# Kernel optimization log

Hardware: AMD Instinct MI355X
Metric: run time of the kernel (lower is better)

Reference implementation:

```python
import jax, jax.numpy as jnp
import numpy as np

TEMPERATURE = 11.313708498984761  # sqrt(128)


def setup_inputs() -> dict:
    key = jax.random.key(0)
    kq, kk, kv = jax.random.split(key, 3)
    b, n, m, d, dv = 16, 2048, 2048, 128, 128
    return {
        "queries": jax.random.normal(kq, (b, n, d), dtype=jnp.float32),
        "keys": jax.random.normal(kk, (b, m, d), dtype=jnp.float32),
        "values": jax.random.normal(kv, (b, m, dv), dtype=jnp.float32),
    }


def reference(queries, keys, values):
    # scores: [b, n, m]
    scores = jnp.einsum('bnd,bmd->bnm', queries, keys) / TEMPERATURE
    attn = jax.nn.softmax(scores, axis=2)
    # out: [b, n, d']
    return jnp.einsum('bnm,bmd->bnd', attn, values)
```

## Files before the change

kernel.cpp:

```cpp
#include <hip/hip_runtime.h>


#define BATCH 16
#define SEQ   2048
#define DIM   128
#define NT    (SEQ / 64)

typedef short bf16x8 __attribute__((ext_vector_type(8)));
typedef float f32x16 __attribute__((ext_vector_type(16)));

static __device__ __forceinline__ unsigned pk2(float lo, float hi) {
  union { float f; unsigned u; } a, b;
  a.f = lo; b.f = hi;
  return ((b.u + 0x8000u) & 0xffff0000u) | ((a.u + 0x8000u) >> 16);
}
static __device__ __forceinline__ float fast_exp2(float x) {
#if __has_builtin(__builtin_amdgcn_exp2f)
  return __builtin_amdgcn_exp2f(x);
#else
  return exp2f(x);
#endif
}

typedef __attribute__((address_space(1))) const unsigned int g_u32;
typedef __attribute__((address_space(3))) unsigned int l_u32;
static __device__ __forceinline__ void gl2lds16(const unsigned short* g, unsigned short* l) {
  __builtin_amdgcn_global_load_lds((g_u32*)g, (l_u32*)l, 16, 0, 0);
}

__global__ __launch_bounds__(256)
void prep_kernel(const float* __restrict__ K, const float* __restrict__ V,
                 unsigned short* __restrict__ Kb, unsigned short* __restrict__ Vt,
                 float scale) {
  const int bx = blockIdx.x, tid = threadIdx.x;
  if (bx < 2048) {
    size_t idx = (size_t)bx * 256 + tid;
    const float4* kf = (const float4*)K;
    float4 a = kf[idx * 2], c = kf[idx * 2 + 1];
    uint4 o;
    o.x = pk2(a.x * scale, a.y * scale);
    o.y = pk2(a.z * scale, a.w * scale);
    o.z = pk2(c.x * scale, c.y * scale);
    o.w = pk2(c.z * scale, c.w * scale);
    ((uint4*)Kb)[idx] = o;
  } else {
    __shared__ float tile[128][33];
    const int vb = bx - 2048;
    const int b = vb >> 6, r = vb & 63;
    const int m0 = (r & 15) * 128, d0 = (r >> 4) * 32;
    const int c = tid & 7, mr = tid >> 3;
    const float* src = V + ((size_t)(b * SEQ) + m0) * DIM + d0;
#pragma unroll
    for (int it = 0; it < 4; ++it) {
      int m = it * 32 + mr;
      float4 x = *(const float4*)(src + (size_t)m * DIM + c * 4);
      tile[m][c * 4 + 0] = x.x; tile[m][c * 4 + 1] = x.y;
      tile[m][c * 4 + 2] = x.z; tile[m][c * 4 + 3] = x.w;
    }
    __syncthreads();
    const int dr = tid >> 3, s = tid & 7;
    unsigned short* dst = Vt + ((size_t)(b * DIM) + d0 + dr) * SEQ + m0;
#pragma unroll
    for (int it = 0; it < 2; ++it) {
      int slot = it * 8 + s;
      uint4 o;
      o.x = pk2(tile[slot * 8 + 0][dr], tile[slot * 8 + 1][dr]);
      o.y = pk2(tile[slot * 8 + 2][dr], tile[slot * 8 + 3][dr]);
      o.z = pk2(tile[slot * 8 + 4][dr], tile[slot * 8 + 5][dr]);
      o.w = pk2(tile[slot * 8 + 6][dr], tile[slot * 8 + 7][dr]);
      *(uint4*)(dst + slot * 8) = o;
    }
  }
}


__global__ __launch_bounds__(256, 2)
void attn_kernel(const float* __restrict__ Qf,
                 const unsigned short* __restrict__ Kb,
                 const unsigned short* __restrict__ Vtb,
                 float* __restrict__ out) {
  __shared__ __align__(1024) unsigned char smem[65536];
  unsigned short* sm16 = (unsigned short*)smem;

  const int tid  = threadIdx.x;
  const int wv   = tid >> 6;
  const int w_q  = wv & 1;
  const int w_m  = wv >> 1;
  const int lane = tid & 63;
  const int l31  = lane & 31;
  const int q2   = lane >> 5;
  const int b    = blockIdx.x;
  const int q0   = blockIdx.y * 64 + w_q * 32;

  const unsigned short* kb = Kb  + (size_t)b * SEQ * DIM;
  const unsigned short* vb = Vtb + (size_t)b * SEQ * DIM;

  bf16x8 aq[8];
  {
    const float* qp = Qf + ((size_t)(b * SEQ) + q0 + l31) * DIM + q2 * 8;
#pragma unroll
    for (int c = 0; c < 8; ++c) {
      float4 x = *(const float4*)(qp + c * 16);
      float4 y = *(const float4*)(qp + c * 16 + 4);
      union { unsigned i[4]; bf16x8 v; } u;
      u.i[0] = pk2(x.x, x.y); u.i[1] = pk2(x.z, x.w);
      u.i[2] = pk2(y.x, y.y); u.i[3] = pk2(y.z, y.w);
      aq[c] = u.v;
    }
  }

  unsigned kgo[4], vgo[4];
#pragma unroll
  for (int i = 0; i < 4; ++i) {
    int ch = wv * 4 + i;
    int krow = ch * 4 + (lane >> 4);
    kgo[i] = (unsigned)(krow * 128) + ((((lane & 15) << 4) ^ ((krow & 15) << 4)) >> 1);
    int vrow = ch * 8 + (lane >> 3);
    vgo[i] = (unsigned)(vrow * 2048) + ((((lane & 7) << 4) ^ ((vrow & 7) << 4)) >> 1);
  }

  const int kro = ((w_m * 32 + l31) << 8) + ((q2 << 4) ^ ((l31 & 15) << 4));
  const int vro = (l31 << 7) + (((w_m << 6) + (q2 << 4)) ^ ((l31 & 7) << 4));

  f32x16 oacc[4];
#pragma unroll
  for (int t = 0; t < 4; ++t)
#pragma unroll
    for (int i = 0; i < 16; ++i) oacc[t][i] = 0.0f;
  float ls[4] = {0.0f, 0.0f, 0.0f, 0.0f};

#define STAGE(TK, BUF) do {                                                  \
    const unsigned short* kt_b = kb + ((size_t)(TK) << 13);                  \
    const unsigned short* vt_b = vb + ((TK) << 6);                           \
    unsigned short* kd = sm16 + (((BUF) + wv * 4096) >> 1);                  \
    unsigned short* vd = sm16 + ((32768 + (BUF) + wv * 4096) >> 1);          \
    _Pragma("unroll")                                                        \
    for (int i = 0; i < 4; ++i) gl2lds16(kt_b + kgo[i], kd + i * 512);       \
    _Pragma("unroll")                                                        \
    for (int i = 0; i < 4; ++i) gl2lds16(vt_b + vgo[i], vd + i * 512);       \
  } while (0)

#define VLOAD(CUR) do {                                                      \
    const unsigned char* vB_ = smem + 32768 + (CUR);                         \
    _Pragma("unroll")                                                        \
    for (int t = 0; t < 4; ++t) {                                            \
      vr[2 * t]     = *(const bf16x8*)(vB_ + t * 4096 + vro);                \
      vr[2 * t + 1] = *(const bf16x8*)(vB_ + t * 4096 + (vro ^ 32));         \
    }                                                                        \
  } while (0)

#define QK(CUR, SD) do {                                                     \
    const unsigned char* kB_ = smem + (CUR);                                 \
    f32x16 se, so;                                                           \
    _Pragma("unroll")                                                        \
    for (int i = 0; i < 16; ++i) { se[i] = 0.0f; so[i] = 0.0f; }             \
    __builtin_amdgcn_s_setprio(1);                                           \
    _Pragma("unroll")                                                        \
    for (int c = 0; c < 4; ++c) {                                            \
      bf16x8 b0 = *(const bf16x8*)(kB_ + (kro ^ ((2 * c) << 5)));            \
      se = __builtin_amdgcn_mfma_f32_32x32x16_bf16(b0, aq[2 * c], se, 0, 0, 0); \
      bf16x8 b1 = *(const bf16x8*)(kB_ + (kro ^ ((2 * c + 1) << 5)));        \
      so = __builtin_amdgcn_mfma_f32_32x32x16_bf16(b1, aq[2 * c + 1], so, 0, 0, 0); \
    }                                                                        \
    __builtin_amdgcn_s_setprio(0);                                           \
    _Pragma("unroll")                                                        \
    for (int i = 0; i < 16; ++i) SD[i] = se[i] + so[i];                      \
  } while (0)

#define SOFTMAX(S, PU0, PU1) do {                                            \
    float p[16];                                                             \
    _Pragma("unroll")                                                        \
    for (int i = 0; i < 16; ++i) p[i] = fast_exp2(S[i]);                     \
    _Pragma("unroll")                                                        \
    for (int i = 0; i < 4; ++i) {                                            \
      ls[0] += p[4 * i + 0]; ls[1] += p[4 * i + 1];                          \
      ls[2] += p[4 * i + 2]; ls[3] += p[4 * i + 3];                          \
    }                                                                        \
    unsigned d0, d1, d2, d3, d4, d5, d6, d7;                                 \
    asm("v_cvt_pk_bf16_f32 %0, %1, %2" : "=v"(d0) : "v"(p[0]),  "v"(p[1]));  \
    asm("v_cvt_pk_bf16_f32 %0, %1, %2" : "=v"(d1) : "v"(p[2]),  "v"(p[3]));  \
    asm("v_cvt_pk_bf16_f32 %0, %1, %2" : "=v"(d2) : "v"(p[4]),  "v"(p[5]));  \
    asm("v_cvt_pk_bf16_f32 %0, %1, %2" : "=v"(d3) : "v"(p[6]),  "v"(p[7]));  \
    asm("v_cvt_pk_bf16_f32 %0, %1, %2" : "=v"(d4) : "v"(p[8]),  "v"(p[9]));  \
    asm("v_cvt_pk_bf16_f32 %0, %1, %2" : "=v"(d5) : "v"(p[10]), "v"(p[11])); \
    asm("v_cvt_pk_bf16_f32 %0, %1, %2" : "=v"(d6) : "v"(p[12]), "v"(p[13])); \
    asm("v_cvt_pk_bf16_f32 %0, %1, %2" : "=v"(d7) : "v"(p[14]), "v"(p[15])); \
    asm("v_permlane32_swap_b32 %0, %1" : "+v"(d0), "+v"(d2));                \
    asm("v_permlane32_swap_b32 %0, %1" : "+v"(d1), "+v"(d3));                \
    asm("v_permlane32_swap_b32 %0, %1" : "+v"(d4), "+v"(d6));                \
    asm("v_permlane32_swap_b32 %0, %1" : "+v"(d5), "+v"(d7));                \
    PU0.u[0] = d0; PU0.u[1] = d1; PU0.u[2] = d2; PU0.u[3] = d3;              \
    PU1.u[0] = d4; PU1.u[1] = d5; PU1.u[2] = d6; PU1.u[3] = d7;              \
  } while (0)

#define PV(PU0, PU1) do {                                                    \
    __builtin_amdgcn_s_setprio(1);                                           \
    _Pragma("unroll")                                                        \
    for (int t = 0; t < 4; ++t) {                                            \
      oacc[t] = __builtin_amdgcn_mfma_f32_32x32x16_bf16(PU0.v, vr[2 * t], oacc[t], 0, 0, 0); \
      oacc[t] = __builtin_amdgcn_mfma_f32_32x32x16_bf16(PU1.v, vr[2 * t + 1], oacc[t], 0, 0, 0); \
    }                                                                        \
    __builtin_amdgcn_s_setprio(0);                                           \
  } while (0)

  bf16x8 vr[8];
  f32x16 sA, sB;

  STAGE(0, 0);
  __syncthreads();
  STAGE(1, 16384);
  QK(0, sA);

#pragma unroll 1
  for (int t = 0; t < NT - 2; t += 2) {
    {
      VLOAD(0);
      __syncthreads();
      STAGE(t + 2, 0);
      QK(16384, sB);
      union { unsigned u[4]; bf16x8 v; } pu0, pu1;
      SOFTMAX(sA, pu0, pu1);
      PV(pu0, pu1);
    }
    {
      VLOAD(16384);
      __syncthreads();
      STAGE(t + 3, 16384);
      QK(0, sA);
      union { unsigned u[4]; bf16x8 v; } pu0, pu1;
      SOFTMAX(sB, pu0, pu1);
      PV(pu0, pu1);
    }
  }
  {
    VLOAD(0);
    __syncthreads();
    QK(16384, sB);
    union { unsigned u[4]; bf16x8 v; } pu0, pu1;
    SOFTMAX(sA, pu0, pu1);
    PV(pu0, pu1);
  }
  {
    VLOAD(16384);
    union { unsigned u[4]; bf16x8 v; } pu0, pu1;
    SOFTMAX(sB, pu0, pu1);
    PV(pu0, pu1);
  }

#undef STAGE
#undef VLOAD
#undef QK
#undef SOFTMAX
#undef PV

  float lsum = (ls[0] + ls[1]) + (ls[2] + ls[3]);
  lsum += __shfl_xor(lsum, 32, 64);

  __syncthreads();
  float* cb  = (float*)smem;
  float* cbL = (float*)(smem + 32768);
  if (w_m == 1) {
    float* my = cb + w_q * 4096;
#pragma unroll
    for (int t = 0; t < 4; ++t)
#pragma unroll
      for (int r = 0; r < 16; ++r)
        my[(t * 16 + r) * 64 + lane] = oacc[t][r];
  }
  cbL[w_m * 64 + w_q * 32 + l31] = lsum;
  __syncthreads();
  if (w_m == 0) {
    const float* pr = cb + w_q * 4096;
    float linv[16];
#pragma unroll
    for (int r = 0; r < 16; ++r) {
      int qr = (r & 3) + ((r >> 2) << 3) + (q2 << 2);
      linv[r] = 1.0f / (cbL[w_q * 32 + qr] + cbL[64 + w_q * 32 + qr]);
    }
    float* ob = out + ((size_t)(b * SEQ) + q0) * DIM;
#pragma unroll
    for (int t = 0; t < 4; ++t)
#pragma unroll
      for (int r = 0; r < 16; ++r) {
        int qr = (r & 3) + ((r >> 2) << 3) + (q2 << 2);
        ob[(size_t)qr * DIM + t * 32 + l31] = (oacc[t][r] + pr[(t * 16 + r) * 64 + lane]) * linv[r];
      }
  }
}

extern "C" void kernel_launch(void* const* d_in, const int* in_sizes, int n_in,
                              void* d_out, int out_size, void* d_ws, size_t ws_size,
                              hipStream_t stream) {
  const float* Q = (const float*)d_in[0];
  const float* K = (const float*)d_in[1];
  const float* V = (const float*)d_in[2];
  float* out = (float*)d_out;

  const size_t elems = (size_t)BATCH * SEQ * DIM;
  unsigned short* Kb = (unsigned short*)d_ws;
  unsigned short* Vt = Kb + elems;

  const double TEMPERATURE = 11.313708498984761;
  const float scale = (float)(1.4426950408889634 / TEMPERATURE);

  prep_kernel<<<3072, 256, 0, stream>>>(K, V, Kb, Vt, scale);
  attn_kernel<<<dim3(BATCH, SEQ / 64), 256, 0, stream>>>(Q, Kb, Vt, out);
}
```

Baseline: 137.8 us.

## Load K directly to registers and triple-buffer V in LDS

K fragments are now read straight from global memory into registers per wave instead of being staged through shared memory. Only V is staged, in a three-slot ring that cuts LDS from 64KB to 48KB. The main loop is restructured so PV for the previous tile runs before QK and softmax for the current one, with a raw s_barrier in place of __syncthreads. This removes K traffic through LDS and may allow more occupancy, but it gives up K reuse across waves (each w_q wave reloads K from global), relies on vmcnt being handled correctly without a full __syncthreads, and may lose the overlap of the two-score-buffer pipeline.

```diff
diff --git a/kernel.cpp b/kernel.cpp
--- a/kernel.cpp
+++ b/kernel.cpp
@@ -79,7 +79,7 @@
                  const unsigned short* __restrict__ Kb,
                  const unsigned short* __restrict__ Vtb,
                  float* __restrict__ out) {
-  __shared__ __align__(1024) unsigned char smem[65536];
+  __shared__ __align__(1024) unsigned char smem[49152];
   unsigned short* sm16 = (unsigned short*)smem;
 
   const int tid  = threadIdx.x;
@@ -109,17 +109,15 @@
     }
   }
 
-  unsigned kgo[4], vgo[4];
+  const unsigned short* kwp = kb + ((size_t)((w_m << 5) + l31) << 7) + (q2 << 3);
+
+  unsigned vgo[4];
 #pragma unroll
   for (int i = 0; i < 4; ++i) {
     int ch = wv * 4 + i;
-    int krow = ch * 4 + (lane >> 4);
-    kgo[i] = (unsigned)(krow * 128) + ((((lane & 15) << 4) ^ ((krow & 15) << 4)) >> 1);
     int vrow = ch * 8 + (lane >> 3);
     vgo[i] = (unsigned)(vrow * 2048) + ((((lane & 7) << 4) ^ ((vrow & 7) << 4)) >> 1);
   }
-
-  const int kro = ((w_m * 32 + l31) << 8) + ((q2 << 4) ^ ((l31 & 15) << 4));
   const int vro = (l31 << 7) + (((w_m << 6) + (q2 << 4)) ^ ((l31 & 7) << 4));
 
   f32x16 oacc[4];
@@ -129,48 +127,35 @@
     for (int i = 0; i < 16; ++i) oacc[t][i] = 0.0f;
   float ls[4] = {0.0f, 0.0f, 0.0f, 0.0f};
 
-#define STAGE(TK, BUF) do {                                                  \
-    const unsigned short* kt_b = kb + ((size_t)(TK) << 13);                  \
-    const unsigned short* vt_b = vb + ((TK) << 6);                           \
-    unsigned short* kd = sm16 + (((BUF) + wv * 4096) >> 1);                  \
-    unsigned short* vd = sm16 + ((32768 + (BUF) + wv * 4096) >> 1);          \
-    _Pragma("unroll")                                                        \
-    for (int i = 0; i < 4; ++i) gl2lds16(kt_b + kgo[i], kd + i * 512);       \
+#define STAGE_V(TV, VOFF) do {                                               \
+    const unsigned short* vt_b = vb + ((TV) << 6);                           \
+    unsigned short* vd = sm16 + (((VOFF) + wv * 4096) >> 1);                 \
     _Pragma("unroll")                                                        \
     for (int i = 0; i < 4; ++i) gl2lds16(vt_b + vgo[i], vd + i * 512);       \
   } while (0)
 
-#define VLOAD(CUR) do {                                                      \
-    const unsigned char* vB_ = smem + 32768 + (CUR);                         \
-    _Pragma("unroll")                                                        \
-    for (int t = 0; t < 4; ++t) {                                            \
-      vr[2 * t]     = *(const bf16x8*)(vB_ + t * 4096 + vro);                \
-      vr[2 * t + 1] = *(const bf16x8*)(vB_ + t * 4096 + (vro ^ 32));         \
-    }                                                                        \
-  } while (0)
-
-#define QK(CUR, SD) do {                                                     \
-    const unsigned char* kB_ = smem + (CUR);                                 \
-    f32x16 se, so;                                                           \
+#define LOADK(TK) do {                                                       \
+    const unsigned short* kp = kwp + ((size_t)(TK) << 13);                   \
+    _Pragma("unroll")                                                        \
+    for (int c = 0; c < 8; ++c) kf[c] = *(const bf16x8*)(kp + c * 16);       \
+  } while (0)
+
+#define QK() do {                                                            \
     _Pragma("unroll")                                                        \
     for (int i = 0; i < 16; ++i) { se[i] = 0.0f; so[i] = 0.0f; }             \
     __builtin_amdgcn_s_setprio(1);                                           \
     _Pragma("unroll")                                                        \
     for (int c = 0; c < 4; ++c) {                                            \
-      bf16x8 b0 = *(const bf16x8*)(kB_ + (kro ^ ((2 * c) << 5)));            \
-      se = __builtin_amdgcn_mfma_f32_32x32x16_bf16(b0, aq[2 * c], se, 0, 0, 0); \
-      bf16x8 b1 = *(const bf16x8*)(kB_ + (kro ^ ((2 * c + 1) << 5)));        \
-      so = __builtin_amdgcn_mfma_f32_32x32x16_bf16(b1, aq[2 * c + 1], so, 0, 0, 0); \
+      se = __builtin_amdgcn_mfma_f32_32x32x16_bf16(kf[2 * c],     aq[2 * c],     se, 0, 0, 0); \
+      so = __builtin_amdgcn_mfma_f32_32x32x16_bf16(kf[2 * c + 1], aq[2 * c + 1], so, 0, 0, 0); \
     }                                                                        \
     __builtin_amdgcn_s_setprio(0);                                           \
-    _Pragma("unroll")                                                        \
-    for (int i = 0; i < 16; ++i) SD[i] = se[i] + so[i];                      \
-  } while (0)
-
-#define SOFTMAX(S, PU0, PU1) do {                                            \
+  } while (0)
+
+#define SOFTMAX() do {                                                       \
     float p[16];                                                             \
     _Pragma("unroll")                                                        \
-    for (int i = 0; i < 16; ++i) p[i] = fast_exp2(S[i]);                     \
+    for (int i = 0; i < 16; ++i) p[i] = fast_exp2(se[i] + so[i]);            \
     _Pragma("unroll")                                                        \
     for (int i = 0; i < 4; ++i) {                                            \
       ls[0] += p[4 * i + 0]; ls[1] += p[4 * i + 1];                          \
@@ -189,66 +174,59 @@
     asm("v_permlane32_swap_b32 %0, %1" : "+v"(d1), "+v"(d3));                \
     asm("v_permlane32_swap_b32 %0, %1" : "+v"(d4), "+v"(d6));                \
     asm("v_permlane32_swap_b32 %0, %1" : "+v"(d5), "+v"(d7));                \
-    PU0.u[0] = d0; PU0.u[1] = d1; PU0.u[2] = d2; PU0.u[3] = d3;              \
-    PU1.u[0] = d4; PU1.u[1] = d5; PU1.u[2] = d6; PU1.u[3] = d7;              \
-  } while (0)
-
-#define PV(PU0, PU1) do {                                                    \
+    pu0.u[0] = d0; pu0.u[1] = d1; pu0.u[2] = d2; pu0.u[3] = d3;              \
+    pu1.u[0] = d4; pu1.u[1] = d5; pu1.u[2] = d6; pu1.u[3] = d7;              \
+  } while (0)
+
+#define PV(VOFF) do {                                                        \
+    const unsigned char* vB_ = smem + (VOFF);                                \
     __builtin_amdgcn_s_setprio(1);                                           \
     _Pragma("unroll")                                                        \
     for (int t = 0; t < 4; ++t) {                                            \
-      oacc[t] = __builtin_amdgcn_mfma_f32_32x32x16_bf16(PU0.v, vr[2 * t], oacc[t], 0, 0, 0); \
-      oacc[t] = __builtin_amdgcn_mfma_f32_32x32x16_bf16(PU1.v, vr[2 * t + 1], oacc[t], 0, 0, 0); \
+      bf16x8 bv0 = *(const bf16x8*)(vB_ + t * 4096 + vro);                   \
+      oacc[t] = __builtin_amdgcn_mfma_f32_32x32x16_bf16(pu0.v, bv0, oacc[t], 0, 0, 0); \
+      bf16x8 bv1 = *(const bf16x8*)(vB_ + t * 4096 + (vro ^ 32));            \
+      oacc[t] = __builtin_amdgcn_mfma_f32_32x32x16_bf16(pu1.v, bv1, oacc[t], 0, 0, 0); \
     }                                                                        \
     __builtin_amdgcn_s_setprio(0);                                           \
   } while (0)
 
-  bf16x8 vr[8];
-  f32x16 sA, sB;
-
-  STAGE(0, 0);
+  bf16x8 kf[8];
+  f32x16 se, so;
+  union { unsigned u[4]; bf16x8 v; } pu0, pu1;
+
+  STAGE_V(0, 0);
+  LOADK(0);
   __syncthreads();
-  STAGE(1, 16384);
-  QK(0, sA);
+  STAGE_V(1, 16384);
+  QK();
+  SOFTMAX();
+
+  int pv_off  = 0;
+  int stg_off = 32768;
 
 #pragma unroll 1
-  for (int t = 0; t < NT - 2; t += 2) {
-    {
-      VLOAD(0);
-      __syncthreads();
-      STAGE(t + 2, 0);
-      QK(16384, sB);
-      union { unsigned u[4]; bf16x8 v; } pu0, pu1;
-      SOFTMAX(sA, pu0, pu1);
-      PV(pu0, pu1);
-    }
-    {
-      VLOAD(16384);
-      __syncthreads();
-      STAGE(t + 3, 16384);
-      QK(0, sA);
-      union { unsigned u[4]; bf16x8 v; } pu0, pu1;
-      SOFTMAX(sB, pu0, pu1);
-      PV(pu0, pu1);
-    }
-  }
-  {
-    VLOAD(0);
-    __syncthreads();
-    QK(16384, sB);
-    union { unsigned u[4]; bf16x8 v; } pu0, pu1;
-    SOFTMAX(sA, pu0, pu1);
-    PV(pu0, pu1);
-  }
-  {
-    VLOAD(16384);
-    union { unsigned u[4]; bf16x8 v; } pu0, pu1;
-    SOFTMAX(sB, pu0, pu1);
-    PV(pu0, pu1);
-  }
-
-#undef STAGE
-#undef VLOAD
+  for (int kt = 1; kt < NT; ++kt) {
+    __builtin_amdgcn_s_barrier();
+    __builtin_amdgcn_sched_barrier(0);
+
+    LOADK(kt);
+    if (kt < NT - 1) STAGE_V(kt + 1, stg_off);
+
+    PV(pv_off);
+    QK();
+    SOFTMAX();
+
+    pv_off  = (pv_off  == 32768) ? 0 : pv_off  + 16384;
+    stg_off = (stg_off == 32768) ? 0 : stg_off + 16384;
+  }
+
+  __builtin_amdgcn_s_barrier();
+  __builtin_amdgcn_sched_barrier(0);
+  PV(16384);
+
+#undef STAGE_V
+#undef LOADK
 #undef QK
 #undef SOFTMAX
 #undef PV
```

Result: slower. 164.3 us (+19.2%).
